# Kernel optimization log

Hardware: AMD Instinct MI355X
Metric: run time of the kernel (lower is better)

## Reference

```python
import jax, jax.numpy as jnp
import numpy as np

# Static sensor configuration (from init_kwargs)
WIDTH = 1024
HEIGHT = 1024
X0, Y0 = -1.0, -1.0
DX = (1.0 - (-1.0)) / WIDTH
DY = (1.0 - (-1.0)) / HEIGHT
SIGMA = 0.1
KERNEL_SIZE = 2

_off = np.arange(-KERNEL_SIZE, KERNEL_SIZE + 1)
_ox, _oy = np.meshgrid(_off, _off, indexing='xy')
OFF_X = jnp.asarray(_ox.flatten(), dtype=jnp.int32)  # [(2k+1)^2] = [25]
OFF_Y = jnp.asarray(_oy.flatten(), dtype=jnp.int32)

N_POINTS = 2_000_000


def setup_inputs() -> dict:
    key = jax.random.key(0)
    k1, k2, k3 = jax.random.split(key, 3)
    x = jax.random.uniform(k1, (N_POINTS,), dtype=jnp.float32)       # in [0,1) subset of bounds
    y = jax.random.uniform(k2, (N_POINTS,), dtype=jnp.float32)
    values = jax.random.normal(k3, (N_POINTS,), dtype=jnp.float32)
    return {"x": x, "y": y, "values": values}


def reference(x, y, values):
    # Map to pixel coordinates
    x_pix = (x - X0) / DX
    y_pix = (y - Y0) / DY
    xi_base = jnp.floor(x_pix).astype(jnp.int32)
    yi_base = jnp.floor(y_pix).astype(jnp.int32)
    x_frac = x_pix - xi_base
    y_frac = y_pix - yi_base

    # [N, 25] neighbor pixel indices and Gaussian weights
    xi = xi_base[:, None] + OFF_X[None, :]
    yi = yi_base[:, None] + OFF_Y[None, :]
    dist_x = x_frac[:, None] - OFF_X[None, :].astype(x_frac.dtype)
    dist_y = y_frac[:, None] - OFF_Y[None, :].astype(y_frac.dtype)
    weights = jnp.exp(-0.5 * (dist_x ** 2 + dist_y ** 2) / (SIGMA ** 2))
    weights = weights / jnp.sum(weights, axis=1, keepdims=True)

    valid = (xi >= 0) & (xi < WIDTH) & (yi >= 0) & (yi < HEIGHT)
    xi = jnp.clip(xi, 0, WIDTH - 1)
    yi = jnp.clip(yi, 0, HEIGHT - 1)

    splatted = values[:, None] * weights * valid  # [N, 25]
    flat_idx = (yi * WIDTH + xi).reshape(-1)      # [N*25]
    img_flat = jax.ops.segment_sum(splatted.reshape(-1), flat_idx,
                                   num_segments=HEIGHT * WIDTH)
    return img_flat.reshape(HEIGHT, WIDTH)
```

## Files before the change

### kernel.cpp

```cpp
#include <hip/hip_runtime.h>
#include <hip/hip_bf16.h>

#define WIDTH 1024
#define HEIGHT 1024
#define IMG_ELEMS (WIDTH * HEIGHT)
#define TPX 32
#define NTILES (TPX * TPX)
#define NB 256
#define BT 1024
#define BSTRIDE 8192
#define CAPP 36
#define PTS_CAP 8448

#define OFF_PTS   0
#define OFF_BIDX  (OFF_PTS + 2 * PTS_CAP)
#define OFF_HCNT  (OFF_BIDX + (NTILES * CAPP) / 2)
#define OFF_RCNT  (OFF_HCNT + NTILES)
#define OFF_RDST  (OFF_RCNT + NB)
#define OFF_ROFF  (OFF_RDST + NB)
#define OFF_STMP  (OFF_ROFF + NB)
#define SMEM_U32  (OFF_STMP + NB)


__device__ __forceinline__ void point_geom(float px, float py, int& cxb, int& cyb,
                                           float& ax, float& ay) {
    float xp = (px + 1.0f) * 512.0f;
    float yp = (py + 1.0f) * 512.0f;
    int xb = (int)floorf(xp);
    int yb = (int)floorf(yp);
    float xf = xp - (float)xb;
    float yf = yp - (float)yb;
    ax = 1.0f / (1.0f + __expf(100.0f * xf - 50.0f));
    ay = 1.0f / (1.0f + __expf(100.0f * yf - 50.0f));
    cxb = min(max(xb, 0), WIDTH - 1);
    cyb = min(max(yb, 0), HEIGHT - 1);
}

__global__ void __launch_bounds__(BT)
k_sortlocal(const float* __restrict__ x, const float* __restrict__ y,
            const float* __restrict__ v, uint2* __restrict__ payload,
            unsigned* __restrict__ runCnt, float4* __restrict__ outv,
            int n, int ppb) {
    __shared__ unsigned cursor[NTILES];
    __shared__ unsigned wtot[BT / 64];
    __shared__ __align__(16) uint2 stage[BSTRIDE];

    int b = blockIdx.x;
    int p = threadIdx.x;
    cursor[p] = 0u;
    outv[(unsigned)b * 1024u + p] = make_float4(0.f, 0.f, 0.f, 0.f);
    __syncthreads();

    int lo = b * ppb;
    int hi = min(n, lo + ppb);

    uint2 pay[8];
    unsigned meta[8];

    auto enc = [&](int s, float px, float py, float pv) {
        int cxb, cyb; float ax, ay;
        point_geom(px, py, cxb, cyb, ax, ay);
        unsigned tile = (unsigned)((cyb >> 5) * TPX + (cxb >> 5));
        unsigned pos = atomicAdd(&cursor[tile], 1u);
        unsigned axq = (unsigned)(ax * 2047.0f + 0.5f);
        unsigned ayq = (unsigned)(ay * 2047.0f + 0.5f);
        pay[s] = make_uint2(__float_as_uint(pv),
                            axq | (ayq << 11) | ((unsigned)(cxb & 31) << 22) |
                            ((unsigned)(cyb & 31) << 27));
        meta[s] = (tile << 16) | pos;
    };

#pragma unroll
    for (int it = 0; it < 2; ++it) {
        int base = lo + p * 4 + it * (BT * 4);
        if (base + 3 < hi) {
            float4 x4 = *(const float4*)&x[base];
            float4 y4 = *(const float4*)&y[base];
            float4 v4 = *(const float4*)&v[base];
            enc(it * 4 + 0, x4.x, y4.x, v4.x);
            enc(it * 4 + 1, x4.y, y4.y, v4.y);
            enc(it * 4 + 2, x4.z, y4.z, v4.z);
            enc(it * 4 + 3, x4.w, y4.w, v4.w);
        } else {
#pragma unroll
            for (int j = 0; j < 4; ++j) {
                int idx = base + j;
                if (idx < hi) enc(it * 4 + j, x[idx], y[idx], v[idx]);
                else          meta[it * 4 + j] = 0xFFFFFFFFu;
            }
        }
    }
    __syncthreads();

    unsigned c = cursor[p];
    unsigned lane = p & 63, w = p >> 6;
    unsigned vsc = c;
#pragma unroll
    for (int d = 1; d < 64; d <<= 1) {
        unsigned t_ = __shfl_up(vsc, d, 64);
        if (lane >= (unsigned)d) vsc += t_;
    }
    if (lane == 63) wtot[w] = vsc;
    __syncthreads();
    if (p == 0) {
        unsigned a = 0;
#pragma unroll
        for (int k = 0; k < BT / 64; ++k) { unsigned t_ = wtot[k]; wtot[k] = a; a += t_; }
    }
    __syncthreads();
    unsigned excl = vsc - c + wtot[w];
    runCnt[(unsigned)b * NTILES + p] = (excl << 16) | c;
    cursor[p] = excl;
    __syncthreads();

#pragma unroll
    for (int s = 0; s < 8; ++s) {
        unsigned m = meta[s];
        if (m != 0xFFFFFFFFu)
            stage[cursor[m >> 16] + (m & 0xFFFFu)] = pay[s];
    }
    __syncthreads();

    int nv = ppb >> 1;
    uint4* dstv = (uint4*)(payload + ((size_t)b << 13));
    const uint4* srcv = (const uint4*)stage;
    for (int i = p; i < nv; i += BT) dstv[i] = srcv[i];
}

__global__ void __launch_bounds__(BT)
k_accum(const uint2* __restrict__ payload, const unsigned* __restrict__ runCnt,
        float* __restrict__ out) {
    __shared__ unsigned smem[SMEM_U32];
    uint2*          pts  = (uint2*)&smem[OFF_PTS];
    unsigned short* bidx = (unsigned short*)&smem[OFF_BIDX];
    unsigned*       hcnt = &smem[OFF_HCNT];
    unsigned*       rcnt = &smem[OFF_RCNT];
    unsigned*       rdst = &smem[OFF_RDST];
    unsigned*       roff = &smem[OFF_ROFF];
    unsigned*       stmp = &smem[OFF_STMP];
    float*          exT01 = (float*)&smem[OFF_PTS];
    float*          exT11 = (float*)&smem[OFF_PTS + BT];

    unsigned b = blockIdx.x;
    unsigned t;
    if (b < 256u) {
        t = (16u + (b >> 4)) * 32u + 16u + (b & 15u);
    } else {
        unsigned r = b - 256u;
        if (r < 512u) t = r;
        else { unsigned q = r - 512u; t = (16u + (q >> 4)) * 32u + (q & 15u); }
    }

    int p = threadIdx.x;
    unsigned lane = p & 63, w = p >> 6;
    unsigned c0 = 0u;
    if (p < NB) {
        unsigned pk = runCnt[(unsigned)p * NTILES + t];
        c0 = pk & 0xFFFFu;
        rcnt[p] = c0;
        roff[p] = pk >> 16;
    }
    hcnt[p] = 0u;
    unsigned tsum = c0;
#pragma unroll
    for (int d = 32; d >= 1; d >>= 1) tsum += __shfl_down(tsum, d, 64);
    if (p < NB && lane == 0) rdst[w] = tsum;
    __syncthreads();
    unsigned total = rdst[0] + rdst[1] + rdst[2] + rdst[3];
    if (total == 0) return;

    unsigned vsc = c0;
#pragma unroll
    for (int d = 1; d < 64; d <<= 1) {
        unsigned tmp = __shfl_up(vsc, d, 64);
        if (lane >= (unsigned)d) vsc += tmp;
    }
    __syncthreads();
    if (p < NB && lane == 63) stmp[w] = vsc;
    __syncthreads();
    if (p == 0) {
        unsigned a = 0;
#pragma unroll
        for (int k = 0; k < 4; ++k) { unsigned tt = stmp[k]; stmp[k] = a; a += tt; }
    }
    __syncthreads();
    if (p < NB) rdst[p] = vsc - c0 + stmp[w];
    __syncthreads();

    unsigned sub = lane >> 3, jl = lane & 7u;
#pragma unroll
    for (int kk = 0; kk < 2; ++kk) {
        int r = (int)w * 16 + kk * 8 + (int)sub;
        unsigned cnt = rcnt[r], dst = rdst[r];
        const unsigned long long* g =
            (const unsigned long long*)(payload + (((size_t)r) << 13) + roff[r]);
        for (unsigned j = jl; j < cnt; j += 8) {
            unsigned long long raw = __builtin_nontemporal_load(&g[j]);
            uint2 pl = make_uint2((unsigned)raw, (unsigned)(raw >> 32));
            unsigned slot = dst + j;
            if (slot < PTS_CAP) {
                pts[slot] = pl;
                unsigned pix = (pl.y >> 22) & 1023u;
                unsigned pos = atomicAdd(&hcnt[pix], 1u);
                if (pos < CAPP) bidx[pix * CAPP + pos] = (unsigned short)slot;
            }
        }
    }
    __syncthreads();

    float t00 = 0.0f, t10 = 0.0f, t01 = 0.0f, t11 = 0.0f;
    unsigned cnt = min(hcnt[p], (unsigned)CAPP);
    for (unsigned e = 0; e < cnt; ++e) {
        uint2 sp = pts[bidx[p * CAPP + e]];
        float val = __uint_as_float(sp.x);
        float ax = (float)(sp.y & 2047u) * (1.0f / 2047.0f);
        float ay = (float)((sp.y >> 11) & 2047u) * (1.0f / 2047.0f);
        float bx = 1.0f - ax, by = 1.0f - ay;
        t00 += val * ax * ay;
        t10 += val * bx * ay;
        t01 += val * ax * by;
        t11 += val * bx * by;
    }
    __syncthreads();
    exT01[p] = t01;
    exT11[p] = t11;
    __syncthreads();

    int lx = p & 31, ly = p >> 5;
    int gx = (int)((t & 31u) << 5) + lx;
    int gy = (int)((t >> 5) << 5) + ly;
    size_t g = (size_t)gy * WIDTH + gx;
    float t10l = __shfl_up(t10, 1, 64);
    float sum = t00;
    if (lx > 0) sum += t10l;
    if (ly > 0) sum += exT01[p - 32];
    if (lx > 0 && ly > 0) sum += exT11[p - 33];
    if (lx == 0 || ly == 0) atomicAdd(&out[g], sum);
    else out[g] = sum;

    bool xr = (gx + 1 < WIDTH), yd = (gy + 1 < HEIGHT);
    if (lx == 31 && xr) {
        atomicAdd(&out[g + 1], t10);
        if (yd) atomicAdd(&out[g + WIDTH + 1], t11);
    }
    if (ly == 31 && yd) {
        atomicAdd(&out[g + WIDTH], t01);
        if (lx < 31 && xr) atomicAdd(&out[g + WIDTH + 1], t11);
    }
}

__global__ void __launch_bounds__(256)
splat_direct(const float* __restrict__ x, const float* __restrict__ y,
             const float* __restrict__ v, float* __restrict__ out, int n) {
    int i = blockIdx.x * blockDim.x + threadIdx.x;
    if (i >= n) return;
    int cxb, cyb; float ax, ay;
    point_geom(x[i], y[i], cxb, cyb, ax, ay);
    float val = v[i];
    float bx = 1.0f - ax, by = 1.0f - ay;
    float* row = out + cyb * WIDTH;
    atomicAdd(row + cxb, val * ax * ay);
    if (cxb + 1 < WIDTH) atomicAdd(row + cxb + 1, val * bx * ay);
    if (cyb + 1 < HEIGHT) {
        row += WIDTH;
        atomicAdd(row + cxb, val * ax * by);
        if (cxb + 1 < WIDTH) atomicAdd(row + cxb + 1, val * bx * by);
    }
}

extern "C" void kernel_launch(void* const* d_in, const int* in_sizes, int n_in,
                              void* d_out, int out_size, void* d_ws, size_t ws_size,
                              hipStream_t stream) {
    const float* x = (const float*)d_in[0];
    const float* y = (const float*)d_in[1];
    const float* v = (const float*)d_in[2];
    float* out = (float*)d_out;
    int n = in_sizes[0];
    int ppb = ((n + NB - 1) / NB + 7) & ~7;

    size_t off_payload = 0;
    size_t off_runcnt  = off_payload + (size_t)NB * BSTRIDE * sizeof(uint2);
    size_t need        = off_runcnt + (size_t)NB * NTILES * sizeof(unsigned);
    bool caps_ok = (ppb <= BSTRIDE) && (out_size == IMG_ELEMS);

    if (ws_size >= need && caps_ok) {
        char* ws = (char*)d_ws;
        uint2*    payload = (uint2*)(ws + off_payload);
        unsigned* runCnt  = (unsigned*)(ws + off_runcnt);

        k_sortlocal<<<NB, BT, 0, stream>>>(x, y, v, payload, runCnt,
                                           (float4*)out, n, ppb);
        k_accum<<<NTILES, BT, 0, stream>>>(payload, runCnt, out);
    } else {
        (void)hipMemsetAsync(out, 0, (size_t)out_size * sizeof(float), stream);
        splat_direct<<<(n + 255) / 256, 256, 0, stream>>>(x, y, v, out, n);
    }
}
```

Before: 95.30 us.

## Replace per-pixel bucketing with direct shared-memory atomic splat in accumulation kernel

The accumulation kernel no longer stages points into shared memory, builds per-pixel bucket lists and then gathers per pixel. Each loaded point now does four shared-memory float atomicAdds into a 33x33 tile image with a halo, and the halo row and column are flushed to global memory with atomics. The runCnt layout is also transposed so each tile's run counts are contiguous, which makes the reads in the accumulation kernel coalesced. This removes a prefix scan, several barriers and the capacity limits (which could drop points), in exchange for contention on shared-memory atomics.

```diff
diff --git a/kernel.cpp b/kernel.cpp
--- a/kernel.cpp
+++ b/kernel.cpp
@@ -9,17 +9,8 @@
 #define NB 256
 #define BT 1024
 #define BSTRIDE 8192
-#define CAPP 36
-#define PTS_CAP 8448
-
-#define OFF_PTS   0
-#define OFF_BIDX  (OFF_PTS + 2 * PTS_CAP)
-#define OFF_HCNT  (OFF_BIDX + (NTILES * CAPP) / 2)
-#define OFF_RCNT  (OFF_HCNT + NTILES)
-#define OFF_RDST  (OFF_RCNT + NB)
-#define OFF_ROFF  (OFF_RDST + NB)
-#define OFF_STMP  (OFF_ROFF + NB)
-#define SMEM_U32  (OFF_STMP + NB)
+#define SIMG_W 33
+#define SIMG_N (SIMG_W * SIMG_W)
 
 
 __device__ __forceinline__ void point_geom(float px, float py, int& cxb, int& cyb,
@@ -109,7 +100,7 @@
     }
     __syncthreads();
     unsigned excl = vsc - c + wtot[w];
-    runCnt[(unsigned)b * NTILES + p] = (excl << 16) | c;
+    runCnt[(unsigned)p * NB + (unsigned)b] = (excl << 16) | c;
     cursor[p] = excl;
     __syncthreads();
 
@@ -130,16 +121,10 @@
 __global__ void __launch_bounds__(BT)
 k_accum(const uint2* __restrict__ payload, const unsigned* __restrict__ runCnt,
         float* __restrict__ out) {
-    __shared__ unsigned smem[SMEM_U32];
-    uint2*          pts  = (uint2*)&smem[OFF_PTS];
-    unsigned short* bidx = (unsigned short*)&smem[OFF_BIDX];
-    unsigned*       hcnt = &smem[OFF_HCNT];
-    unsigned*       rcnt = &smem[OFF_RCNT];
-    unsigned*       rdst = &smem[OFF_RDST];
-    unsigned*       roff = &smem[OFF_ROFF];
-    unsigned*       stmp = &smem[OFF_STMP];
-    float*          exT01 = (float*)&smem[OFF_PTS];
-    float*          exT11 = (float*)&smem[OFF_PTS + BT];
+    __shared__ float simg[SIMG_N];
+    __shared__ unsigned rcnt[NB];
+    __shared__ unsigned roff[NB];
+    __shared__ unsigned wsum[4];
 
     unsigned b = blockIdx.x;
     unsigned t;
@@ -155,97 +140,67 @@
     unsigned lane = p & 63, w = p >> 6;
     unsigned c0 = 0u;
     if (p < NB) {
-        unsigned pk = runCnt[(unsigned)p * NTILES + t];
+        unsigned pk = runCnt[t * NB + (unsigned)p];
         c0 = pk & 0xFFFFu;
         rcnt[p] = c0;
         roff[p] = pk >> 16;
     }
-    hcnt[p] = 0u;
+    simg[p] = 0.0f;
+    if (p < SIMG_N - BT) simg[BT + p] = 0.0f;
     unsigned tsum = c0;
 #pragma unroll
     for (int d = 32; d >= 1; d >>= 1) tsum += __shfl_down(tsum, d, 64);
-    if (p < NB && lane == 0) rdst[w] = tsum;
-    __syncthreads();
-    unsigned total = rdst[0] + rdst[1] + rdst[2] + rdst[3];
+    if (p < NB && lane == 0) wsum[w] = tsum;
+    __syncthreads();
+    unsigned total = wsum[0] + wsum[1] + wsum[2] + wsum[3];
     if (total == 0) return;
-
-    unsigned vsc = c0;
-#pragma unroll
-    for (int d = 1; d < 64; d <<= 1) {
-        unsigned tmp = __shfl_up(vsc, d, 64);
-        if (lane >= (unsigned)d) vsc += tmp;
-    }
-    __syncthreads();
-    if (p < NB && lane == 63) stmp[w] = vsc;
-    __syncthreads();
-    if (p == 0) {
-        unsigned a = 0;
-#pragma unroll
-        for (int k = 0; k < 4; ++k) { unsigned tt = stmp[k]; stmp[k] = a; a += tt; }
-    }
-    __syncthreads();
-    if (p < NB) rdst[p] = vsc - c0 + stmp[w];
-    __syncthreads();
 
     unsigned sub = lane >> 3, jl = lane & 7u;
 #pragma unroll
     for (int kk = 0; kk < 2; ++kk) {
         int r = (int)w * 16 + kk * 8 + (int)sub;
-        unsigned cnt = rcnt[r], dst = rdst[r];
+        unsigned cnt = rcnt[r];
         const unsigned long long* g =
             (const unsigned long long*)(payload + (((size_t)r) << 13) + roff[r]);
         for (unsigned j = jl; j < cnt; j += 8) {
             unsigned long long raw = __builtin_nontemporal_load(&g[j]);
-            uint2 pl = make_uint2((unsigned)raw, (unsigned)(raw >> 32));
-            unsigned slot = dst + j;
-            if (slot < PTS_CAP) {
-                pts[slot] = pl;
-                unsigned pix = (pl.y >> 22) & 1023u;
-                unsigned pos = atomicAdd(&hcnt[pix], 1u);
-                if (pos < CAPP) bidx[pix * CAPP + pos] = (unsigned short)slot;
-            }
-        }
-    }
-    __syncthreads();
-
-    float t00 = 0.0f, t10 = 0.0f, t01 = 0.0f, t11 = 0.0f;
-    unsigned cnt = min(hcnt[p], (unsigned)CAPP);
-    for (unsigned e = 0; e < cnt; ++e) {
-        uint2 sp = pts[bidx[p * CAPP + e]];
-        float val = __uint_as_float(sp.x);
-        float ax = (float)(sp.y & 2047u) * (1.0f / 2047.0f);
-        float ay = (float)((sp.y >> 11) & 2047u) * (1.0f / 2047.0f);
-        float bx = 1.0f - ax, by = 1.0f - ay;
-        t00 += val * ax * ay;
-        t10 += val * bx * ay;
-        t01 += val * ax * by;
-        t11 += val * bx * by;
-    }
-    __syncthreads();
-    exT01[p] = t01;
-    exT11[p] = t11;
+            unsigned plo = (unsigned)raw, phi = (unsigned)(raw >> 32);
+            float val = __uint_as_float(plo);
+            float ax = (float)(phi & 2047u) * (1.0f / 2047.0f);
+            float ay = (float)((phi >> 11) & 2047u) * (1.0f / 2047.0f);
+            unsigned lx = (phi >> 22) & 31u;
+            unsigned ly = phi >> 27;
+            float bx = 1.0f - ax, by = 1.0f - ay;
+            float vay = val * ay, vby = val * by;
+            unsigned base = ly * SIMG_W + lx;
+            atomicAdd(&simg[base],              vay * ax);
+            atomicAdd(&simg[base + 1],          vay * bx);
+            atomicAdd(&simg[base + SIMG_W],     vby * ax);
+            atomicAdd(&simg[base + SIMG_W + 1], vby * bx);
+        }
+    }
     __syncthreads();
 
     int lx = p & 31, ly = p >> 5;
-    int gx = (int)((t & 31u) << 5) + lx;
-    int gy = (int)((t >> 5) << 5) + ly;
-    size_t g = (size_t)gy * WIDTH + gx;
-    float t10l = __shfl_up(t10, 1, 64);
-    float sum = t00;
-    if (lx > 0) sum += t10l;
-    if (ly > 0) sum += exT01[p - 32];
-    if (lx > 0 && ly > 0) sum += exT11[p - 33];
-    if (lx == 0 || ly == 0) atomicAdd(&out[g], sum);
-    else out[g] = sum;
-
-    bool xr = (gx + 1 < WIDTH), yd = (gy + 1 < HEIGHT);
-    if (lx == 31 && xr) {
-        atomicAdd(&out[g + 1], t10);
-        if (yd) atomicAdd(&out[g + WIDTH + 1], t11);
-    }
-    if (ly == 31 && yd) {
-        atomicAdd(&out[g + WIDTH], t01);
-        if (lx < 31 && xr) atomicAdd(&out[g + WIDTH + 1], t11);
+    int gx0 = (int)((t & 31u) << 5), gy0 = (int)((t >> 5) << 5);
+    size_t g = (size_t)(gy0 + ly) * WIDTH + gx0 + lx;
+    float s = simg[ly * SIMG_W + lx];
+    if (lx == 0 || ly == 0) atomicAdd(&out[g], s);
+    else out[g] = s;
+
+    if (p < 32) {
+        if (gx0 + 32 < WIDTH) {
+            float hv = simg[p * SIMG_W + 32];
+            if (hv != 0.0f)
+                atomicAdd(&out[(size_t)(gy0 + p) * WIDTH + gx0 + 32], hv);
+        }
+    } else if (p < 65) {
+        int c = p - 32;
+        if (gy0 + 32 < HEIGHT && gx0 + c < WIDTH) {
+            float hv = simg[32 * SIMG_W + c];
+            if (hv != 0.0f)
+                atomicAdd(&out[(size_t)(gy0 + 32) * WIDTH + gx0 + c], hv);
+        }
     }
 }
 
```

Measured after the change: 125.5 us. +31.7%, slower.
